# Kernel optimization log

Hardware: AMD Instinct MI355X
Metric: run time of the kernel (lower is better)

The kernel has to match this reference:

```python
import jax, jax.numpy as jnp
import numpy as np

B, L, IN, H, W = 4096, 10, 8, 512, 512


def setup_inputs() -> dict:
    key = jax.random.key(0)
    ks = jax.random.split(key, 24)
    s = 0.05  # small init so tanh/sigmoid stay in active range
    def rn(k, shape):
        return jax.random.normal(k, shape, dtype=jnp.float32) * s
    return {
        "items": jax.random.normal(ks[0], (B, L, IN), dtype=jnp.float32),
        "decoder_items_input": jax.random.uniform(ks[1], (B, H), dtype=jnp.float32),
        "emb_w": rn(ks[2], (H, IN)), "emb_b": rn(ks[3], (H,)),
        "enc_wih": rn(ks[4], (3 * H, H)), "enc_whh": rn(ks[5], (3 * H, H)),
        "enc_bih": rn(ks[6], (3 * H,)), "enc_bhh": rn(ks[7], (3 * H,)),
        "dec_wih": rn(ks[8], (3 * H, H)), "dec_whh": rn(ks[9], (3 * H, H)),
        "dec_bih": rn(ks[10], (3 * H,)), "dec_bhh": rn(ks[11], (3 * H,)),
        "w1": rn(ks[12], (W, H)), "w2": rn(ks[13], (W, H)),
        "w3": rn(ks[14], (W, H)), "w4": rn(ks[15], (W, H)),
        "w5": rn(ks[16], (W, H)), "w6": rn(ks[17], (W, H)),
        "w7": rn(ks[18], (W, 2 * H)),
        "v1": rn(ks[19], (W,)), "v2": rn(ks[20], (W,)),
        "v3_w": rn(ks[21], (W,)), "v3_b": rn(ks[22], (1,)),
        "wori": rn(ks[23], (6, 3 * H)), "bori": jnp.zeros((6,), jnp.float32),
    }


def _gru_scan(xg, whh, bhh, h0):
    # xg: [L,B,3H] precomputed input-gate projections; returns all hidden states [L,B,H]
    def step(h, xg_t):
        hg = h @ whh.T + bhh
        xr, xz, xn = jnp.split(xg_t, 3, axis=-1)
        hr, hz, hn = jnp.split(hg, 3, axis=-1)
        r = jax.nn.sigmoid(xr + hr)
        z = jax.nn.sigmoid(xz + hz)
        n = jnp.tanh(xn + r * hn)
        h_new = (1.0 - z) * n + z * h
        return h_new, h_new
    _, ys = jax.lax.scan(step, h0, xg)
    return ys


def _forward(items, decoder_items_input, emb_w, emb_b, enc_wih, enc_whh, enc_bih, enc_bhh,
             dec_wih, dec_whh, dec_bih, dec_bhh, w1, w2, w3, w4, w5, w6, w7,
             v1, v2, v3_w, v3_b, wori, bori):
    Bsz, Lln, _ = items.shape
    Hh = emb_w.shape[0]
    x = items @ emb_w.T + emb_b                                  # [B,L,H] embedding
    xg = (x @ enc_wih.T + enc_bih).transpose(1, 0, 2)            # [L,B,3H]
    enc_out = _gru_scan(xg, enc_whh, enc_bhh, jnp.zeros((Bsz, Hh), x.dtype))  # [L,B,H]
    h0 = enc_out[-1]                                             # last encoder state
    enc_blh = enc_out.transpose(1, 0, 2)                         # [B,L,H]
    enc_w3 = enc_out @ w3.T                                      # [L,B,W] (hoisted, step-invariant)
    enc_w6 = enc_out @ w6.T                                      # [L,B,W]
    xg_dec = decoder_items_input @ dec_wih.T + dec_bih           # [B,3H] constant decoder input
    xr, xz, xn = jnp.split(xg_dec, 3, axis=-1)

    def step(h, _):
        hg = h @ dec_whh.T + dec_bhh
        hr, hz, hn = jnp.split(hg, 3, axis=-1)
        r = jax.nn.sigmoid(xr + hr)
        z = jax.nn.sigmoid(xz + hz)
        n = jnp.tanh(xn + r * hn)
        h_new = (1.0 - z) * n + z * h                            # GRUCell update
        # intra attention cache is always length-1 in the source (the shape[1]==1 branch
        # always fires), so log_softmax is over a singleton axis -> exactly zero.
        doi = h_new[:, None, :]                                  # [B,1,H]
        oi = jnp.tanh(h_new @ w1.T + h_new @ w2.T) @ v1          # [B]
        attnd = jax.nn.log_softmax(oi[:, None, None], axis=-1)   # [B,1,1] zeros
        hi = (attnd * doi).sum(axis=1)                           # [B,H] (zeros, faithful)
        sm = jnp.tanh(enc_w3 + h_new @ w4.T + hi @ w5.T)         # [L,B,W]
        out_seq = (sm @ v2).T                                    # [B,L]
        sm_ori = jnp.tanh(enc_w6 + jnp.concatenate([h_new, hi], axis=-1) @ w7.T)  # [L,B,W]
        oo = sm_ori @ v3_w + v3_b[0]                             # [L,B]
        attnc = jax.nn.log_softmax(oo.T[:, :, None], axis=-1)    # [B,L,1] zeros (singleton axis)
        he = (attnc * enc_blh).sum(axis=1)                       # [B,H]
        total = jnp.concatenate([he, h_new, hi], axis=-1)        # [B,3H]
        out_ori = total @ wori.T + bori                          # [B,6]
        return h_new, (out_seq, out_ori)

    _, (seqs, oris) = jax.lax.scan(step, h0, None, length=Lln)
    probs_seq = seqs.transpose(1, 0, 2)                          # [B,L,L]
    probs_ori = oris.transpose(1, 0, 2)                          # [B,L,6]
    return probs_seq, probs_ori


def reference(items, decoder_items_input, emb_w, emb_b, enc_wih, enc_whh, enc_bih, enc_bhh,
              dec_wih, dec_whh, dec_bih, dec_bhh, w1, w2, w3, w4, w5, w6, w7,
              v1, v2, v3_w, v3_b, wori, bori):
    return _forward(items, decoder_items_input, emb_w, emb_b, enc_wih, enc_whh, enc_bih,
                    enc_bhh, dec_wih, dec_whh, dec_bih, dec_bhh, w1, w2, w3, w4, w5, w6,
                    w7, v1, v2, v3_w, v3_b, wori, bori)
```

## Files before the change

### kernel.cpp

```cpp
#include <hip/hip_runtime.h>
#include <hip/hip_bf16.h>


#define B_   4096
#define L_   10
#define IN_  8
#define H_   512
#define H3_  1536
#define W_   512
#define ORI_BASE (B_ * L_ * L_)

typedef __attribute__((ext_vector_type(8))) short s8v;
typedef __attribute__((ext_vector_type(4))) float f4v;

#define LOG2E  1.4426950408889634f
#define LOG2E2 2.8853900817779268f

__device__ __forceinline__ float sig_fast(float x) {
  float e = __builtin_amdgcn_exp2f(-x * LOG2E);
  return __builtin_amdgcn_rcpf(1.f + e);
}
__device__ __forceinline__ float tanh_fast(float x) {
  float e = __builtin_amdgcn_exp2f(x * LOG2E2);
  return 1.f - 2.f * __builtin_amdgcn_rcpf(e + 1.f);
}
__device__ __forceinline__ short f2bf(float f) {
  __hip_bfloat16 h = __float2bfloat16(f);
  return __builtin_bit_cast(short, h);
}
__device__ __forceinline__ float bf2f(short s) {
  __hip_bfloat16 h = __builtin_bit_cast(__hip_bfloat16, s);
  return __bfloat162float(h);
}
__device__ __forceinline__ void stc(float* p, float v) { *p = v; }
__device__ __forceinline__ void stc(short* p, float v) { *p = f2bf(v); }

__global__ __launch_bounds__(256) void f2bf_k(const float* __restrict__ src,
                                              short* __restrict__ dst, int n)
{
  int i = blockIdx.x * 256 + threadIdx.x;
  if (i < n) dst[i] = f2bf(src[i]);
}

__global__ __launch_bounds__(256) void build_wc(
    const float* __restrict__ enc_wih, const float* __restrict__ emb_w,
    const float* __restrict__ emb_b, const float* __restrict__ enc_bih,
    float* __restrict__ Wc, float* __restrict__ bc)
{
  __shared__ float se[H_ * IN_];
  __shared__ float sb[H_];
  const int tid = threadIdx.x;
  for (int i = tid; i < H_ * IN_; i += 256) se[i] = emb_w[i];
  for (int i = tid; i < H_; i += 256) sb[i] = emb_b[i];
  __syncthreads();
  int g = (blockIdx.x * 256 + tid) >> 6;
  int lane = tid & 63;
  const float* wr = enc_wih + (long)g * H_ + lane * 8;
  float w8[8];
#pragma unroll
  for (int j = 0; j < 8; ++j) w8[j] = wr[j];
  float acc[9] = {};
#pragma unroll
  for (int kk = 0; kk < 8; ++kk) {
    int k = lane * 8 + kk;
#pragma unroll
    for (int j = 0; j < 8; ++j) acc[j] += w8[kk] * se[k * IN_ + j];
    acc[8] += w8[kk] * sb[k];
  }
#pragma unroll
  for (int j = 0; j < 9; ++j)
#pragma unroll
    for (int off = 32; off; off >>= 1) acc[j] += __shfl_down(acc[j], off, 64);
  if (lane == 0) {
#pragma unroll
    for (int j = 0; j < 8; ++j) Wc[g * IN_ + j] = acc[j];
    bc[g] = acc[8] + enc_bih[g];
  }
}

template <typename CT>
__global__ __launch_bounds__(256) void gemm_bf16(
    const short* __restrict__ A, long lda,
    const short* __restrict__ Bw, long ldb,
    const float* __restrict__ bias,
    CT* __restrict__ C, long ldc, int K, float scale)
{
  __shared__ short As[128 * 32];
  __shared__ short Bs[128 * 32];
  const int tid = threadIdx.x;
  const long row0 = (long)blockIdx.y * 128;
  const long col0 = (long)blockIdx.x * 128;
  const int wave = tid >> 6, lane = tid & 63;
  const int wm = (wave & 1) * 64, wn = (wave >> 1) * 64;
  const int r16 = lane & 15, quad = lane >> 4;
  f4v acc[4][4] = {};

  for (int k0 = 0; k0 < K; k0 += 32) {
#pragma unroll
    for (int r = 0; r < 2; ++r) {
      int idx = r * 256 + tid;
      int m = idx >> 2;
      int k8 = (idx & 3) * 8;
      __builtin_amdgcn_global_load_lds(
          (const __attribute__((address_space(1))) void*)(A + (row0 + m) * lda + k0 + k8),
          (__attribute__((address_space(3))) void*)(As + idx * 8), 16, 0, 0);
      __builtin_amdgcn_global_load_lds(
          (const __attribute__((address_space(1))) void*)(Bw + (col0 + m) * ldb + k0 + k8),
          (__attribute__((address_space(3))) void*)(Bs + idx * 8), 16, 0, 0);
    }
    __syncthreads();
    s8v af[4], bf[4];
#pragma unroll
    for (int i = 0; i < 4; ++i)
      af[i] = *(const s8v*)&As[(wm + i * 16 + r16) * 32 + quad * 8];
#pragma unroll
    for (int j = 0; j < 4; ++j)
      bf[j] = *(const s8v*)&Bs[(wn + j * 16 + r16) * 32 + quad * 8];
#pragma unroll
    for (int i = 0; i < 4; ++i)
#pragma unroll
      for (int j = 0; j < 4; ++j)
        acc[i][j] = __builtin_amdgcn_mfma_f32_16x16x32_bf16(af[i], bf[j], acc[i][j], 0, 0, 0);
    __syncthreads();
  }

#pragma unroll
  for (int i = 0; i < 4; ++i) {
    long rbase = row0 + wm + i * 16 + quad * 4;
#pragma unroll
    for (int j = 0; j < 4; ++j) {
      long c = col0 + wn + j * 16 + r16;
      float bv = bias ? bias[c] : 0.f;
#pragma unroll
      for (int rg = 0; rg < 4; ++rg)
        stc(&C[(rbase + rg) * ldc + c], (acc[i][j][rg] + bv) * scale);
    }
  }
}

template <bool ENC>
__global__ __launch_bounds__(256) void gru_fused(
    const short* __restrict__ Aprev,
    const short* __restrict__ Whh,
    const float* __restrict__ bhh,
    const short* __restrict__ xg,
    const float* __restrict__ items_t,
    const float* __restrict__ Wc,
    const float* __restrict__ bc,
    float* __restrict__ h,
    short* __restrict__ hout)
{
  __shared__ short As[2][64 * 64];
  __shared__ short Bs[2][192 * 64];
  const int tid = threadIdx.x;
  const long row0 = (long)blockIdx.y * 64;
  const int col0 = blockIdx.x * 64;
  const int wave = tid >> 6, lane = tid & 63;
  const int r16 = lane & 15, quad = lane >> 4;
  const int sw = r16 & 7;

  f4v acc[3][4] = {};

  auto stage = [&](int buf, int k0) {
#pragma unroll
    for (int r = 0; r < 2; ++r) {
      int idx = r * 256 + tid;
      int m = idx >> 3, c8 = idx & 7;
      int src = c8 ^ (m & 7);
      __builtin_amdgcn_global_load_lds(
          (const __attribute__((address_space(1))) void*)(Aprev + (row0 + m) * H_ + k0 + src * 8),
          (__attribute__((address_space(3))) void*)(&As[buf][idx * 8]), 16, 0, 0);
    }
#pragma unroll
    for (int r = 0; r < 6; ++r) {
      int idx = r * 256 + tid;
      int m = idx >> 3, c8 = idx & 7;
      int src = c8 ^ (m & 7);
      int g = m >> 6, cc = m & 63;
      __builtin_amdgcn_global_load_lds(
          (const __attribute__((address_space(1))) void*)(Whh + ((long)g * H_ + col0 + cc) * H_ + k0 + src * 8),
          (__attribute__((address_space(3))) void*)(&Bs[buf][idx * 8]), 16, 0, 0);
    }
  };

  stage(0, 0);
  int cur = 0;
  for (int k = 0; k < 8; ++k) {
    if (k < 7) {
      stage(cur ^ 1, (k + 1) * 64);
      asm volatile("s_waitcnt vmcnt(8)" ::: "memory");
    } else {
      asm volatile("s_waitcnt vmcnt(0)" ::: "memory");
    }
    __builtin_amdgcn_s_barrier();
    s8v af[4][2], bf[3][2];
#pragma unroll
    for (int i = 0; i < 4; ++i)
#pragma unroll
      for (int hh = 0; hh < 2; ++hh)
        af[i][hh] = *(const s8v*)&As[cur][(i * 16 + r16) * 64 + ((hh * 4 + quad) ^ sw) * 8];
#pragma unroll
    for (int g = 0; g < 3; ++g)
#pragma unroll
      for (int hh = 0; hh < 2; ++hh)
        bf[g][hh] = *(const s8v*)&Bs[cur][(g * 64 + wave * 16 + r16) * 64 + ((hh * 4 + quad) ^ sw) * 8];
    __builtin_amdgcn_s_setprio(1);
#pragma unroll
    for (int hh = 0; hh < 2; ++hh)
#pragma unroll
      for (int g = 0; g < 3; ++g)
#pragma unroll
        for (int i = 0; i < 4; ++i)
          acc[g][i] = __builtin_amdgcn_mfma_f32_16x16x32_bf16(af[i][hh], bf[g][hh], acc[g][i], 0, 0, 0);
    __builtin_amdgcn_s_setprio(0);
    __builtin_amdgcn_s_barrier();
    cur ^= 1;
  }

  const int col = col0 + wave * 16 + r16;
  float wc[3][8], bcv[3];
  if (ENC) {
#pragma unroll
    for (int g = 0; g < 3; ++g) {
      const float* wr = Wc + ((long)g * H_ + col) * IN_;
#pragma unroll
      for (int j = 0; j < 8; ++j) wc[g][j] = wr[j];
      bcv[g] = bc[g * H_ + col];
    }
    float* itemS = (float*)As;
    int i2 = tid * 2;
    int m = i2 >> 3, j = i2 & 7;
    itemS[i2] = items_t[(row0 + m) * (L_ * IN_) + j];
    itemS[i2 + 1] = items_t[(row0 + m) * (L_ * IN_) + j + 1];
    __syncthreads();
  }
  float bhr = bhh[col], bhz = bhh[col + H_], bhn = bhh[col + 2 * H_];

#pragma unroll
  for (int i = 0; i < 4; ++i) {
#pragma unroll
    for (int rg = 0; rg < 4; ++rg) {
      int rl = i * 16 + quad * 4 + rg;
      long row = row0 + rl;
      float xr, xz, xn;
      if (ENC) {
        const float* it = (const float*)As + rl * 8;
        xr = bcv[0]; xz = bcv[1]; xn = bcv[2];
#pragma unroll
        for (int j = 0; j < 8; ++j) {
          float iv = it[j];
          xr += iv * wc[0][j];
          xz += iv * wc[1][j];
          xn += iv * wc[2][j];
        }
      } else {
        long gx = row * H3_ + col;
        xr = bf2f(xg[gx]); xz = bf2f(xg[gx + H_]); xn = bf2f(xg[gx + 2 * H_]);
      }
      float r = sig_fast(xr + acc[0][i][rg] + bhr);
      float z = sig_fast(xz + acc[1][i][rg] + bhz);
      float n = tanh_fast(xn + r * (acc[2][i][rg] + bhn));
      long hi = row * H_ + col;
      float hv = (1.f - z) * n + z * h[hi];
      h[hi] = hv;
      hout[hi] = f2bf(hv);
    }
  }
}

__global__ __launch_bounds__(256) void out_seq_all(
    const short* __restrict__ ew3,
    const short* __restrict__ a4,
    const float* __restrict__ v2,
    float* __restrict__ out)
{
  __shared__ float se[L_ * W_];
  __shared__ float sa[L_ * W_];
  const int b = blockIdx.x;
  const int tid = threadIdx.x;
  for (int i = tid; i < L_ * W_ / 8; i += 256) {
    int l = i >> 6, c = i & 63;
    s8v ev = *(const s8v*)(ew3 + ((long)l * B_ + b) * W_ + c * 8);
    s8v av = *(const s8v*)(a4 + ((long)l * B_ + b) * W_ + c * 8);
    f4v e0, e1, a0, a1;
#pragma unroll
    for (int j = 0; j < 4; ++j) {
      e0[j] = bf2f(ev[j]); e1[j] = bf2f(ev[j + 4]);
      a0[j] = bf2f(av[j]); a1[j] = bf2f(av[j + 4]);
    }
    *(f4v*)(se + i * 8) = e0; *(f4v*)(se + i * 8 + 4) = e1;
    *(f4v*)(sa + i * 8) = a0; *(f4v*)(sa + i * 8 + 4) = a1;
  }
  const int wave = tid >> 6, lane = tid & 63;
  float svp[8], svtot = 0.f;
#pragma unroll
  for (int j = 0; j < 8; ++j) {
    float v = v2[lane * 8 + j];
    svp[j] = -2.f * v;
    svtot += v;
  }
#pragma unroll
  for (int off = 32; off; off >>= 1) svtot += __shfl_down(svtot, off, 64);
  __syncthreads();

#pragma unroll
  for (int pp = 0; pp < 25; ++pp) {
    int p = wave * 25 + pp;
    int t = p / L_, l = p - t * L_;
    const float* ep = se + l * W_ + lane * 8;
    const float* ap = sa + t * W_ + lane * 8;
    f4v e0 = *(const f4v*)ep, e1 = *(const f4v*)(ep + 4);
    f4v a0 = *(const f4v*)ap, a1 = *(const f4v*)(ap + 4);
    float acc = 0.f;
#pragma unroll
    for (int j = 0; j < 4; ++j) {
      float x0 = __builtin_amdgcn_exp2f(e0[j] + a0[j]);
      acc += svp[j] * __builtin_amdgcn_rcpf(x0 + 1.f);
      float x1 = __builtin_amdgcn_exp2f(e1[j] + a1[j]);
      acc += svp[j + 4] * __builtin_amdgcn_rcpf(x1 + 1.f);
    }
#pragma unroll
    for (int off = 32; off; off >>= 1) acc += __shfl_down(acc, off, 64);
    if (lane == 0) out[((long)b * L_ + t) * L_ + l] = svtot + acc;
  }
}

__global__ __launch_bounds__(256) void out_ori_all(
    const short* __restrict__ dh,
    const float* __restrict__ wori, const float* __restrict__ bori,
    float* __restrict__ out)
{
  int wid = (blockIdx.x * 256 + threadIdx.x) >> 6;
  int lane = threadIdx.x & 63;
  int b = wid / L_, t = wid - b * L_;
  s8v hv = *(const s8v*)(dh + ((long)t * B_ + b) * H_ + lane * 8);
  float hf[8];
#pragma unroll
  for (int j = 0; j < 8; ++j) hf[j] = bf2f(hv[j]);
  float res[6];
#pragma unroll
  for (int o = 0; o < 6; ++o) {
    const float* wr = wori + (long)o * H3_ + H_ + lane * 8;
    float acc = 0.f;
#pragma unroll
    for (int j = 0; j < 8; ++j) acc += hf[j] * wr[j];
#pragma unroll
    for (int off = 32; off; off >>= 1) acc += __shfl_down(acc, off, 64);
    res[o] = acc;
  }
  if (lane == 0) {
    float* po = out + ORI_BASE + ((long)b * L_ + t) * 6;
#pragma unroll
    for (int o = 0; o < 6; ++o) po[o] = res[o] + bori[o];
  }
}

extern "C" void kernel_launch(void* const* d_in, const int* in_sizes, int n_in,
                              void* d_out, int out_size, void* d_ws, size_t ws_size,
                              hipStream_t stream)
{
  const float* items   = (const float*)d_in[0];
  const float* dec_in  = (const float*)d_in[1];
  const float* emb_w   = (const float*)d_in[2];
  const float* emb_b   = (const float*)d_in[3];
  const float* enc_wih = (const float*)d_in[4];
  const float* enc_whh = (const float*)d_in[5];
  const float* enc_bih = (const float*)d_in[6];
  const float* enc_bhh = (const float*)d_in[7];
  const float* dec_wih = (const float*)d_in[8];
  const float* dec_whh = (const float*)d_in[9];
  const float* dec_bih = (const float*)d_in[10];
  const float* dec_bhh = (const float*)d_in[11];
  const float* w3      = (const float*)d_in[14];
  const float* w4      = (const float*)d_in[15];
  const float* v2      = (const float*)d_in[20];
  const float* wori    = (const float*)d_in[23];
  const float* bori    = (const float*)d_in[24];
  float* out = (float*)d_out;

  char* ws = (char*)d_ws;
  size_t off = 0;
  auto alloc = [&](size_t bytes) { size_t o = off; off += (bytes + 255) & ~255UL; return o; };
  float* Wc       = (float*)(ws + alloc(H3_ * IN_ * 4));
  float* bc       = (float*)(ws + alloc(H3_ * 4));
  float* h        = (float*)(ws + alloc((size_t)B_ * H_ * 4));
  short* xgb      = (short*)(ws + alloc((size_t)B_ * H3_ * 2));
  short* enc_hist = (short*)(ws + alloc((size_t)11 * B_ * H_ * 2));
  short* dec_hist = (short*)(ws + alloc((size_t)L_ * B_ * H_ * 2));
  short* ew3      = (short*)(ws + alloc((size_t)L_ * B_ * W_ * 2));
  short* a4       = (short*)(ws + alloc((size_t)L_ * B_ * W_ * 2));
  short* whh_e    = (short*)(ws + alloc((size_t)H3_ * H_ * 2));
  short* whh_d    = (short*)(ws + alloc((size_t)H3_ * H_ * 2));
  short* wih_d    = (short*)(ws + alloc((size_t)H3_ * H_ * 2));
  short* w3b      = (short*)(ws + alloc((size_t)W_ * H_ * 2));
  short* w4b      = (short*)(ws + alloc((size_t)W_ * H_ * 2));
  short* decb     = (short*)(ws + alloc((size_t)B_ * H_ * 2));

  f2bf_k<<<(H3_ * H_ + 255) / 256, 256, 0, stream>>>(enc_whh, whh_e, H3_ * H_);
  f2bf_k<<<(H3_ * H_ + 255) / 256, 256, 0, stream>>>(dec_whh, whh_d, H3_ * H_);
  f2bf_k<<<(H3_ * H_ + 255) / 256, 256, 0, stream>>>(dec_wih, wih_d, H3_ * H_);
  f2bf_k<<<(W_ * H_ + 255) / 256, 256, 0, stream>>>(w3, w3b, W_ * H_);
  f2bf_k<<<(W_ * H_ + 255) / 256, 256, 0, stream>>>(w4, w4b, W_ * H_);
  f2bf_k<<<(B_ * H_ + 255) / 256, 256, 0, stream>>>(dec_in, decb, B_ * H_);
  build_wc<<<384, 256, 0, stream>>>(enc_wih, emb_w, emb_b, enc_bih, Wc, bc);

  hipMemsetAsync(h, 0, (size_t)B_ * H_ * 4, stream);
  hipMemsetAsync(enc_hist, 0, (size_t)B_ * H_ * 2, stream);

  for (int t = 0; t < L_; ++t) {
    gru_fused<true><<<dim3(8, 64), 256, 0, stream>>>(
        enc_hist + (size_t)t * B_ * H_, whh_e, enc_bhh, nullptr,
        items + (size_t)t * IN_, Wc, bc, h,
        enc_hist + (size_t)(t + 1) * B_ * H_);
  }

  gemm_bf16<short><<<dim3(12, 32), 256, 0, stream>>>(
      decb, H_, wih_d, H_, dec_bih, xgb, H3_, H_, 1.f);

  for (int t = 0; t < L_; ++t) {
    const short* prev = (t == 0) ? enc_hist + (size_t)10 * B_ * H_
                                 : dec_hist + (size_t)(t - 1) * B_ * H_;
    gru_fused<false><<<dim3(8, 64), 256, 0, stream>>>(
        prev, whh_d, dec_bhh, xgb, nullptr, nullptr, nullptr, h,
        dec_hist + (size_t)t * B_ * H_);
  }

  gemm_bf16<short><<<dim3(4, 320), 256, 0, stream>>>(
      enc_hist + (size_t)B_ * H_, H_, w3b, H_, nullptr, ew3, W_, H_, LOG2E2);
  gemm_bf16<short><<<dim3(4, 320), 256, 0, stream>>>(
      dec_hist, H_, w4b, H_, nullptr, a4, W_, H_, LOG2E2);
  out_seq_all<<<B_, 256, 0, stream>>>(ew3, a4, v2, out);
  out_ori_all<<<(B_ * L_) / 4, 256, 0, stream>>>(dec_hist, wori, bori, out);
}
```

Baseline: 632.4 us.

## Double-buffer bf16 GEMM with swizzled LDS, fuse conversions, retile out_seq loads

The bf16 GEMM now uses a 64-wide K tile with double-buffered LDS, XOR-swizzled columns to avoid bank conflicts, explicit vmcnt waits and raised MFMA priority, so global loads overlap compute. The six separate fp32-to-bf16 conversion launches are merged into one vectorized kernel. out_seq_all uses a 4-element interleaved layout and reuses the attention row across consecutive pairs. The decoder input GEMM is moved before the encoder loop. These mainly cut launch overhead and GEMM latency, at the cost of more LDS use per block.

```diff
diff --git a/kernel.cpp b/kernel.cpp
--- a/kernel.cpp
+++ b/kernel.cpp
@@ -11,6 +11,7 @@
 #define ORI_BASE (B_ * L_ * L_)
 
 typedef __attribute__((ext_vector_type(8))) short s8v;
+typedef __attribute__((ext_vector_type(4))) short s4v;
 typedef __attribute__((ext_vector_type(4))) float f4v;
 
 #define LOG2E  1.4426950408889634f
@@ -35,11 +36,28 @@
 __device__ __forceinline__ void stc(float* p, float v) { *p = v; }
 __device__ __forceinline__ void stc(short* p, float v) { *p = f2bf(v); }
 
-__global__ __launch_bounds__(256) void f2bf_k(const float* __restrict__ src,
-                                              short* __restrict__ dst, int n)
-{
-  int i = blockIdx.x * 256 + threadIdx.x;
-  if (i < n) dst[i] = f2bf(src[i]);
+__global__ __launch_bounds__(256) void prep_all(
+    const float* __restrict__ s0, short* __restrict__ d0,
+    const float* __restrict__ s1, short* __restrict__ d1,
+    const float* __restrict__ s2, short* __restrict__ d2,
+    const float* __restrict__ s3, short* __restrict__ d3,
+    const float* __restrict__ s4, short* __restrict__ d4,
+    const float* __restrict__ s5, short* __restrict__ d5)
+{
+  long i8 = (long)blockIdx.x * 256 + threadIdx.x;
+  const float* s; short* d; long off;
+  if      (i8 < 98304)  { s = s0; d = d0; off = i8; }
+  else if (i8 < 196608) { s = s1; d = d1; off = i8 - 98304; }
+  else if (i8 < 294912) { s = s2; d = d2; off = i8 - 196608; }
+  else if (i8 < 327680) { s = s3; d = d3; off = i8 - 294912; }
+  else if (i8 < 360448) { s = s4; d = d4; off = i8 - 327680; }
+  else if (i8 < 622592) { s = s5; d = d5; off = i8 - 360448; }
+  else return;
+  const float* sp = s + off * 8;
+  s8v v;
+#pragma unroll
+  for (int j = 0; j < 8; ++j) v[j] = f2bf(sp[j]);
+  *(s8v*)(d + off * 8) = v;
 }
 
 __global__ __launch_bounds__(256) void build_wc(
@@ -85,43 +103,71 @@
     const float* __restrict__ bias,
     CT* __restrict__ C, long ldc, int K, float scale)
 {
-  __shared__ short As[128 * 32];
-  __shared__ short Bs[128 * 32];
+  __shared__ short As[2][128 * 64];
+  __shared__ short Bs[2][128 * 64];
   const int tid = threadIdx.x;
   const long row0 = (long)blockIdx.y * 128;
   const long col0 = (long)blockIdx.x * 128;
   const int wave = tid >> 6, lane = tid & 63;
   const int wm = (wave & 1) * 64, wn = (wave >> 1) * 64;
   const int r16 = lane & 15, quad = lane >> 4;
+  const int sw = r16 & 7;
   f4v acc[4][4] = {};
 
-  for (int k0 = 0; k0 < K; k0 += 32) {
-#pragma unroll
-    for (int r = 0; r < 2; ++r) {
+  auto stage = [&](int buf, int k0) {
+#pragma unroll
+    for (int r = 0; r < 4; ++r) {
       int idx = r * 256 + tid;
-      int m = idx >> 2;
-      int k8 = (idx & 3) * 8;
+      int m = idx >> 3, c8 = idx & 7;
+      int src = c8 ^ (m & 7);
       __builtin_amdgcn_global_load_lds(
-          (const __attribute__((address_space(1))) void*)(A + (row0 + m) * lda + k0 + k8),
-          (__attribute__((address_space(3))) void*)(As + idx * 8), 16, 0, 0);
+          (const __attribute__((address_space(1))) void*)(A + (row0 + m) * lda + k0 + src * 8),
+          (__attribute__((address_space(3))) void*)(&As[buf][idx * 8]), 16, 0, 0);
+    }
+#pragma unroll
+    for (int r = 0; r < 4; ++r) {
+      int idx = r * 256 + tid;
+      int m = idx >> 3, c8 = idx & 7;
+      int src = c8 ^ (m & 7);
       __builtin_amdgcn_global_load_lds(
-          (const __attribute__((address_space(1))) void*)(Bw + (col0 + m) * ldb + k0 + k8),
-          (__attribute__((address_space(3))) void*)(Bs + idx * 8), 16, 0, 0);
-    }
-    __syncthreads();
-    s8v af[4], bf[4];
+          (const __attribute__((address_space(1))) void*)(Bw + (col0 + m) * ldb + k0 + src * 8),
+          (__attribute__((address_space(3))) void*)(&Bs[buf][idx * 8]), 16, 0, 0);
+    }
+  };
+
+  const int nk = K >> 6;
+  stage(0, 0);
+  for (int k = 0; k < nk; ++k) {
+    if (k < nk - 1) {
+      stage((k + 1) & 1, (k + 1) * 64);
+      asm volatile("s_waitcnt vmcnt(8)" ::: "memory");
+    } else {
+      asm volatile("s_waitcnt vmcnt(0)" ::: "memory");
+    }
+    __builtin_amdgcn_s_barrier();
+    const short* Asc = As[k & 1];
+    const short* Bsc = Bs[k & 1];
+    s8v af[4][2], bf[4][2];
 #pragma unroll
     for (int i = 0; i < 4; ++i)
-      af[i] = *(const s8v*)&As[(wm + i * 16 + r16) * 32 + quad * 8];
+#pragma unroll
+      for (int hh = 0; hh < 2; ++hh)
+        af[i][hh] = *(const s8v*)&Asc[(wm + i * 16 + r16) * 64 + ((hh * 4 + quad) ^ sw) * 8];
 #pragma unroll
     for (int j = 0; j < 4; ++j)
-      bf[j] = *(const s8v*)&Bs[(wn + j * 16 + r16) * 32 + quad * 8];
-#pragma unroll
-    for (int i = 0; i < 4; ++i)
-#pragma unroll
-      for (int j = 0; j < 4; ++j)
-        acc[i][j] = __builtin_amdgcn_mfma_f32_16x16x32_bf16(af[i], bf[j], acc[i][j], 0, 0, 0);
-    __syncthreads();
+#pragma unroll
+      for (int hh = 0; hh < 2; ++hh)
+        bf[j][hh] = *(const s8v*)&Bsc[(wn + j * 16 + r16) * 64 + ((hh * 4 + quad) ^ sw) * 8];
+    __builtin_amdgcn_s_setprio(1);
+#pragma unroll
+    for (int hh = 0; hh < 2; ++hh)
+#pragma unroll
+      for (int i = 0; i < 4; ++i)
+#pragma unroll
+        for (int j = 0; j < 4; ++j)
+          acc[i][j] = __builtin_amdgcn_mfma_f32_16x16x32_bf16(af[i][hh], bf[j][hh], acc[i][j], 0, 0, 0);
+    __builtin_amdgcn_s_setprio(0);
+    __builtin_amdgcn_s_barrier();
   }
 
 #pragma unroll
@@ -278,46 +324,50 @@
   __shared__ float sa[L_ * W_];
   const int b = blockIdx.x;
   const int tid = threadIdx.x;
-  for (int i = tid; i < L_ * W_ / 8; i += 256) {
-    int l = i >> 6, c = i & 63;
-    s8v ev = *(const s8v*)(ew3 + ((long)l * B_ + b) * W_ + c * 8);
-    s8v av = *(const s8v*)(a4 + ((long)l * B_ + b) * W_ + c * 8);
-    f4v e0, e1, a0, a1;
-#pragma unroll
-    for (int j = 0; j < 4; ++j) {
-      e0[j] = bf2f(ev[j]); e1[j] = bf2f(ev[j + 4]);
-      a0[j] = bf2f(av[j]); a1[j] = bf2f(av[j + 4]);
-    }
-    *(f4v*)(se + i * 8) = e0; *(f4v*)(se + i * 8 + 4) = e1;
-    *(f4v*)(sa + i * 8) = a0; *(f4v*)(sa + i * 8 + 4) = a1;
+  for (int i = tid; i < L_ * 128; i += 256) {
+    int row = i >> 7, q = i & 127;
+    s4v ev = *(const s4v*)(ew3 + ((long)row * B_ + b) * W_ + q * 4);
+    s4v av = *(const s4v*)(a4 + ((long)row * B_ + b) * W_ + q * 4);
+    f4v e, a;
+#pragma unroll
+    for (int j = 0; j < 4; ++j) { e[j] = bf2f(ev[j]); a[j] = bf2f(av[j]); }
+    *(f4v*)(se + row * W_ + q * 4) = e;
+    *(f4v*)(sa + row * W_ + q * 4) = a;
   }
   const int wave = tid >> 6, lane = tid & 63;
-  float svp[8], svtot = 0.f;
-#pragma unroll
-  for (int j = 0; j < 8; ++j) {
-    float v = v2[lane * 8 + j];
-    svp[j] = -2.f * v;
-    svtot += v;
+  float sv0[4], sv1[4], svtot = 0.f;
+#pragma unroll
+  for (int q = 0; q < 4; ++q) {
+    float v = v2[lane * 4 + q];
+    sv0[q] = -2.f * v; svtot += v;
+    v = v2[256 + lane * 4 + q];
+    sv1[q] = -2.f * v; svtot += v;
   }
 #pragma unroll
   for (int off = 32; off; off >>= 1) svtot += __shfl_down(svtot, off, 64);
+  svtot = __shfl(svtot, 0, 64);
   __syncthreads();
 
+  int tprev = -1;
+  f4v a0, a1;
 #pragma unroll
   for (int pp = 0; pp < 25; ++pp) {
     int p = wave * 25 + pp;
     int t = p / L_, l = p - t * L_;
-    const float* ep = se + l * W_ + lane * 8;
-    const float* ap = sa + t * W_ + lane * 8;
-    f4v e0 = *(const f4v*)ep, e1 = *(const f4v*)(ep + 4);
-    f4v a0 = *(const f4v*)ap, a1 = *(const f4v*)(ap + 4);
+    if (t != tprev) {
+      a0 = *(const f4v*)(sa + t * W_ + lane * 4);
+      a1 = *(const f4v*)(sa + t * W_ + 256 + lane * 4);
+      tprev = t;
+    }
+    f4v e0 = *(const f4v*)(se + l * W_ + lane * 4);
+    f4v e1 = *(const f4v*)(se + l * W_ + 256 + lane * 4);
     float acc = 0.f;
 #pragma unroll
-    for (int j = 0; j < 4; ++j) {
-      float x0 = __builtin_amdgcn_exp2f(e0[j] + a0[j]);
-      acc += svp[j] * __builtin_amdgcn_rcpf(x0 + 1.f);
-      float x1 = __builtin_amdgcn_exp2f(e1[j] + a1[j]);
-      acc += svp[j + 4] * __builtin_amdgcn_rcpf(x1 + 1.f);
+    for (int q = 0; q < 4; ++q) {
+      float x0 = __builtin_amdgcn_exp2f(e0[q] + a0[q]);
+      acc += sv0[q] * __builtin_amdgcn_rcpf(x0 + 1.f);
+      float x1 = __builtin_amdgcn_exp2f(e1[q] + a1[q]);
+      acc += sv1[q] * __builtin_amdgcn_rcpf(x1 + 1.f);
     }
 #pragma unroll
     for (int off = 32; off; off >>= 1) acc += __shfl_down(acc, off, 64);
@@ -396,16 +446,16 @@
   short* w4b      = (short*)(ws + alloc((size_t)W_ * H_ * 2));
   short* decb     = (short*)(ws + alloc((size_t)B_ * H_ * 2));
 
-  f2bf_k<<<(H3_ * H_ + 255) / 256, 256, 0, stream>>>(enc_whh, whh_e, H3_ * H_);
-  f2bf_k<<<(H3_ * H_ + 255) / 256, 256, 0, stream>>>(dec_whh, whh_d, H3_ * H_);
-  f2bf_k<<<(H3_ * H_ + 255) / 256, 256, 0, stream>>>(dec_wih, wih_d, H3_ * H_);
-  f2bf_k<<<(W_ * H_ + 255) / 256, 256, 0, stream>>>(w3, w3b, W_ * H_);
-  f2bf_k<<<(W_ * H_ + 255) / 256, 256, 0, stream>>>(w4, w4b, W_ * H_);
-  f2bf_k<<<(B_ * H_ + 255) / 256, 256, 0, stream>>>(dec_in, decb, B_ * H_);
+  prep_all<<<(622592 + 255) / 256, 256, 0, stream>>>(
+      enc_whh, whh_e, dec_whh, whh_d, dec_wih, wih_d,
+      w3, w3b, w4, w4b, dec_in, decb);
   build_wc<<<384, 256, 0, stream>>>(enc_wih, emb_w, emb_b, enc_bih, Wc, bc);
 
   hipMemsetAsync(h, 0, (size_t)B_ * H_ * 4, stream);
   hipMemsetAsync(enc_hist, 0, (size_t)B_ * H_ * 2, stream);
+
+  gemm_bf16<short><<<dim3(12, 32), 256, 0, stream>>>(
+      decb, H_, wih_d, H_, dec_bih, xgb, H3_, H_, 1.f);
 
   for (int t = 0; t < L_; ++t) {
     gru_fused<true><<<dim3(8, 64), 256, 0, stream>>>(
@@ -413,9 +463,6 @@
         items + (size_t)t * IN_, Wc, bc, h,
         enc_hist + (size_t)(t + 1) * B_ * H_);
   }
-
-  gemm_bf16<short><<<dim3(12, 32), 256, 0, stream>>>(
-      decb, H_, wih_d, H_, dec_bih, xgb, H3_, H_, 1.f);
 
   for (int t = 0; t < L_; ++t) {
     const short* prev = (t == 0) ? enc_hist + (size_t)10 * B_ * H_
```

Measured after the change: 602.5 us. -4.7%, faster.
